# Kernel optimization log

Measured on AMD Instinct MI355X. Metric: run time of the kernel, lower is better.

The kernel has to match this reference:

```python
import jax, jax.numpy as jnp
import numpy as np

TAU = 1.0  # temperature of the NeuralSort relaxation


def _neural_sort(s, tau=TAU):
    """NeuralSort soft permutation matrix for scores s of shape (n,).
    Returns (n, n) row-stochastic matrix; row i ~ one-hot of i-th largest score."""
    n = s.shape[0]
    A_sum = jnp.abs(s[:, None] - s[None, :]).sum(-1)              # (n,)
    scaling = (n + 1 - 2 * jnp.arange(1, n + 1)).astype(s.dtype)  # (n,)
    scores = (scaling[:, None] * s[None, :] - A_sum[None, :]) / tau
    return jax.nn.softmax(scores, axis=-1)


def _soft_perm_gt(events, d):
    """Vectorized version of _get_soft_perm.
    events: (n,) int {0,1}; d: (n,) float durations. Returns (n, n) float32."""
    n = events.shape[0]
    idx = jnp.argsort(d)                 # ascending durations
    e_s = events[idx]                    # events in sorted order
    c = jnp.cumsum(e_s) - e_s            # exclusive event count before position i
    i = jnp.arange(n)
    lo = c                               # first allowed rank column
    hi = jnp.where(e_s == 1, i + 1, n)   # one past last allowed rank column
    j = jnp.arange(n)
    mask = (j[None, :] >= lo[:, None]) & (j[None, :] < hi[:, None])
    rows = mask.astype(jnp.float32) / (hi - lo)[:, None].astype(jnp.float32)
    inv = jnp.argsort(idx)               # perm_un_ascending @ M == rows re-indexed
    return rows[inv]


def _bce(p, y):
    # torch BCELoss: clamp log terms at -100, mean over all elements
    logp = jnp.maximum(jnp.log(p), -100.0)
    log1mp = jnp.maximum(jnp.log1p(-p), -100.0)
    return -(y * logp + (1.0 - y) * log1mp).mean()


def setup_inputs() -> dict:
    key = jax.random.key(0)
    k1, k2, k3 = jax.random.split(key, 3)
    n, C = 2048, 8
    logits = jax.random.normal(k1, (n, C), dtype=jnp.float32)
    durations = jax.random.uniform(k2, (n, C), dtype=jnp.float32)
    events = jax.random.randint(k3, (n, C), 0, 2).astype(jnp.int32)
    return {"logits": logits, "events": events, "durations": durations}


def reference(logits, events, durations):
    def col_loss(lh, e, d):
        p = _neural_sort(lh)        # (n, n) soft permutation prediction
        y = _soft_perm_gt(e, d)     # (n, n) soft permutation label
        return _bce(p, y)

    losses = jax.vmap(col_loss, in_axes=(1, 1, 1))(logits, events, durations)  # (C,)
    m = losses > 0
    denom = jnp.maximum(jnp.sum(m), 1).astype(losses.dtype)
    return jnp.sum(jnp.where(m, losses, 0.0)) / denom
```

## Files before the change

kernel.cpp:

```cpp
#include <hip/hip_runtime.h>
#include <hip/hip_bf16.h>
#include <math.h>

#define N 2048
#define NC 8


#if __has_builtin(__builtin_amdgcn_exp2f)
__device__ __forceinline__ float fexp2(float x) { return __builtin_amdgcn_exp2f(x); }
#else
__device__ __forceinline__ float fexp2(float x) { return exp2f(x); }
#endif
#if __has_builtin(__builtin_amdgcn_logf)
__device__ __forceinline__ float flog2(float x) { return __builtin_amdgcn_logf(x); }
#else
__device__ __forceinline__ float flog2(float x) { return log2f(x); }
#endif

#define INV_LN2 1.4426950408889634f
#define LN2_D   0.6931471805599453
#define CLAMP2  (-144.26950408889634f)

__global__ __launch_bounds__(256) void k_prep(const float* __restrict__ logits,
                                              const float* __restrict__ dur,
                                              const int* __restrict__ ev,
                                              float2* __restrict__ psort,
                                              unsigned short* __restrict__ origj,
                                              int* __restrict__ lohi,
                                              double* __restrict__ acc,
                                              unsigned* __restrict__ counter) {
    __shared__ __align__(16) float s[N];
    __shared__ double part[256];
    __shared__ int pri[256];
    __shared__ __align__(16) unsigned long long keys[N];
    __shared__ int pr[256], pv[256];

    int b = blockIdx.x;
    int tid = threadIdx.x;

    if (b == 0) {
        if (tid < 8) acc[tid] = 0.0;
        else if (tid == 8) counter[0] = 0u;
    }

    if (b < 512) {
        int col = b >> 6, chunk = b & 63;
        for (int k = 0; k < N / 256; ++k) {
            int i = tid + k * 256;
            s[i] = logits[i * NC + col];
        }
        __syncthreads();
        int jl = tid & 31, slice = tid >> 5;
        int j = chunk * 32 + jl;
        float sj = s[j];
        const float4* s4 = (const float4*)(s + slice * 256);
        int ib = slice * 256;
        double a0 = 0.0, a1 = 0.0, a2 = 0.0, a3 = 0.0;
        int rk = 0;
        #pragma unroll 8
        for (int i = 0; i < 64; ++i) {
            float4 q = s4[i];
            int i0 = ib + 4 * i;
            a0 += (double)fabsf(sj - q.x);
            a1 += (double)fabsf(sj - q.y);
            a2 += (double)fabsf(sj - q.z);
            a3 += (double)fabsf(sj - q.w);
            rk += ((int)(q.x < sj)) | (((int)(q.x == sj)) & (int)(i0 + 0 < j));
            rk += ((int)(q.y < sj)) | (((int)(q.y == sj)) & (int)(i0 + 1 < j));
            rk += ((int)(q.z < sj)) | (((int)(q.z == sj)) & (int)(i0 + 2 < j));
            rk += ((int)(q.w < sj)) | (((int)(q.w == sj)) & (int)(i0 + 3 < j));
        }
        part[tid] = (a0 + a1) + (a2 + a3);
        pri[tid] = rk;
        __syncthreads();
        if (tid < 32) {
            double v = ((part[tid]       + part[tid + 32])  + (part[tid + 64]  + part[tid + 96])) +
                       ((part[tid + 128] + part[tid + 160]) + (part[tid + 192] + part[tid + 224]));
            int r = ((pri[tid]       + pri[tid + 32])  + (pri[tid + 64]  + pri[tid + 96])) +
                    ((pri[tid + 128] + pri[tid + 160]) + (pri[tid + 192] + pri[tid + 224]));
            psort[col * N + r] = make_float2(sj * INV_LN2, (float)v * INV_LN2);
            origj[col * N + r] = (unsigned short)j;
        }
    } else {
        int b2 = b - 512;
        int col = b2 >> 6, chunk = b2 & 63;
        for (int k = 0; k < N / 256; ++k) {
            int i = tid + k * 256;
            unsigned int db = __float_as_uint(dur[i * NC + col]);
            int e = ev[i * NC + col];
            keys[i] = ((unsigned long long)db << 32) | (unsigned int)((i << 1) | e);
        }
        __syncthreads();
        int jl = tid & 31, slice = tid >> 5;
        int j = chunk * 32 + jl;
        unsigned long long kj = keys[j];
        const ulonglong2* k2 = (const ulonglong2*)(keys + slice * 256);
        int rank = 0, evlt = 0;
        #pragma unroll 8
        for (int i = 0; i < 128; ++i) {
            ulonglong2 kk = k2[i];
            int lt0 = (kk.x < kj) ? 1 : 0;
            rank += lt0;
            evlt += lt0 & (int)(kk.x & 1ull);
            int lt1 = (kk.y < kj) ? 1 : 0;
            rank += lt1;
            evlt += lt1 & (int)(kk.y & 1ull);
        }
        pr[tid] = rank;
        pv[tid] = evlt;
        __syncthreads();
        if (tid < 32) {
            int r = ((pr[tid]       + pr[tid + 32])  + (pr[tid + 64]  + pr[tid + 96])) +
                    ((pr[tid + 128] + pr[tid + 160]) + (pr[tid + 192] + pr[tid + 224]));
            int v = ((pv[tid]       + pv[tid + 32])  + (pv[tid + 64]  + pv[tid + 96])) +
                    ((pv[tid + 128] + pv[tid + 160]) + (pv[tid + 192] + pv[tid + 224]));
            int e = (int)(kj & 1ull);
            int hi = e ? (r + 1) : N;
            lohi[col * N + j] = v | (hi << 16);
        }
    }
}

__global__ __launch_bounds__(512) void k_bce(const float2* __restrict__ psort,
                                             const unsigned short* __restrict__ origj,
                                             const int* __restrict__ lohi,
                                             double* __restrict__ acc,
                                             unsigned* __restrict__ counter,
                                             float* __restrict__ out) {
    int col = blockIdx.x >> 6;
    int rg  = blockIdx.x & 63;
    __shared__ float4 sa4[N / 2];
    __shared__ unsigned sow[N / 2];
    __shared__ double bsum[8];
    int tid = threadIdx.x;
    int wave = tid >> 6, lane = tid & 63;

    const float4* p4 = (const float4*)(psort + (size_t)col * N);
    const unsigned* g4 = (const unsigned*)(origj + (size_t)col * N);
    #pragma unroll
    for (int k = 0; k < 2; ++k) {
        int i = tid + (k << 9);
        sa4[i] = p4[i];
        sow[i] = g4[i];
    }
    __syncthreads();

    int row0 = (rg << 5) + (wave << 2);
    float sc0 = (float)(N - 1 - 2 * row0);

    int lh[4];
    #pragma unroll
    for (int c = 0; c < 4; ++c) lh[c] = lohi[col * N + row0 + c];

    float m = -INFINITY;
    #pragma unroll
    for (int k = 0; k < 16; ++k) {
        float4 q = sa4[lane + (k << 6)];
        float t0 = fmaf(sc0, q.x, -q.y);
        float t1 = fmaf(sc0, q.z, -q.w);
        m = fmaxf(m, fmaxf(t0, t1));
    }
    #pragma unroll
    for (int off = 32; off > 0; off >>= 1)
        m = fmaxf(m, __shfl_xor(m, off, 64));

    float se0 = 0.0f, se1 = 0.0f, se2 = 0.0f, se3 = 0.0f;
    #pragma unroll
    for (int kg = 0; kg < 2; ++kg) {
        float4 qv[8];
        #pragma unroll
        for (int t = 0; t < 8; ++t)
            qv[t] = sa4[lane + (((kg << 3) | t) << 6)];
        #pragma unroll
        for (int t = 0; t < 8; ++t) {
            float4 q = qv[t];
            float tsa = q.x + q.x;
            float xa0 = fmaf(sc0, q.x, -q.y) - m;
            float xa3 = fmaf(-3.0f, tsa, xa0);
            float tsb = q.z + q.z;
            float xb0 = fmaf(sc0, q.z, -q.w) - m;
            float xb3 = fmaf(-3.0f, tsb, xb0);
            float hi = fmaxf(fmaxf(xa0, xa3), fmaxf(xb0, xb3));
            if (__all(hi < -152.0f)) continue;
            float xa1 = xa0 - tsa;
            float xa2 = fmaf(-2.0f, tsa, xa0);
            float xb1 = xb0 - tsb;
            float xb2 = fmaf(-2.0f, tsb, xb0);
            se0 += fexp2(xa0); se1 += fexp2(xa1); se2 += fexp2(xa2); se3 += fexp2(xa3);
            se0 += fexp2(xb0); se1 += fexp2(xb1); se2 += fexp2(xb2); se3 += fexp2(xb3);
        }
    }
    #pragma unroll
    for (int off = 32; off > 0; off >>= 1) {
        se0 += __shfl_xor(se0, off, 64);
        se1 += __shfl_xor(se1, off, 64);
        se2 += __shfl_xor(se2, off, 64);
        se3 += __shfl_xor(se3, off, 64);
    }
    float se[4] = {se0, se1, se2, se3};

    float L2v[4], C2v[4], yv[4], w2c[4];
    unsigned lo[4], wl[4];
    double rbase = 0.0;
    #pragma unroll
    for (int c = 0; c < 4; ++c) {
        float L2 = flog2(se[c]);
        L2v[c] = L2;
        rbase -= 2048.0 * (double)L2;
        C2v[c] = CLAMP2 + L2;
        w2c[c] = C2v[c] - L2v[c];
        lo[c] = (unsigned)(lh[c] & 0xffff);
        wl[c] = (unsigned)((lh[c] >> 16) & 0xffff) - lo[c];
        yv[c] = 1.0f / (float)wl[c];
    }
    float minL2 = fminf(fminf(L2v[0], L2v[1]), fminf(L2v[2], L2v[3]));
    float C2min = fminf(fminf(C2v[0], C2v[1]), fminf(C2v[2], C2v[3]));
    float tdeep = fminf(C2min, minL2 - 27.0f);
    float t2    = minL2 - 27.0f;

    float a1[4] = {0.0f, 0.0f, 0.0f, 0.0f};
    float a2[4] = {0.0f, 0.0f, 0.0f, 0.0f};
    int cntD[4] = {0, 0, 0, 0};
    int nL = 0;
    #pragma unroll
    for (int kg = 0; kg < 2; ++kg) {
        float4 qv[8];
        unsigned owv[8];
        #pragma unroll
        for (int t = 0; t < 8; ++t) {
            int idx = lane + (((kg << 3) | t) << 6);
            qv[t] = sa4[idx];
            owv[t] = sow[idx];
        }
        #pragma unroll
        for (int t = 0; t < 8; ++t) {
            float4 q = qv[t];
            unsigned ow = owv[t];
            int ja = (int)(ow & 0xffffu), jb = (int)(ow >> 16);
            float tsa = q.x + q.x;
            float xa0 = fmaf(sc0, q.x, -q.y) - m;
            float xa3 = fmaf(-3.0f, tsa, xa0);
            float tsb = q.z + q.z;
            float xb0 = fmaf(sc0, q.z, -q.w) - m;
            float xb3 = fmaf(-3.0f, tsb, xb0);
            float hi = fmaxf(fmaxf(xa0, xa3), fmaxf(xb0, xb3));
            if (__all(hi < tdeep)) {
                ++nL;
                #pragma unroll
                for (int c = 0; c < 4; ++c) {
                    cntD[c] += (int)((unsigned)(ja - lo[c]) < wl[c]);
                    cntD[c] += (int)((unsigned)(jb - lo[c]) < wl[c]);
                }
            } else if (__all(hi < t2)) {
                ++nL;
                {
                    float x = xa0;
                    #pragma unroll
                    for (int c = 0; c < 4; ++c) {
                        float mx1 = fmaxf(x, C2v[c]);
                        float w = ((unsigned)(ja - lo[c]) < wl[c]) ? (mx1 - L2v[c]) : 0.0f;
                        a2[c] += w;
                        x -= tsa;
                    }
                }
                {
                    float x = xb0;
                    #pragma unroll
                    for (int c = 0; c < 4; ++c) {
                        float mx1 = fmaxf(x, C2v[c]);
                        float w = ((unsigned)(jb - lo[c]) < wl[c]) ? (mx1 - L2v[c]) : 0.0f;
                        a2[c] += w;
                        x -= tsb;
                    }
                }
            } else {
                float xav[4], xbv[4];
                xav[0] = xa0; xav[1] = xa0 - tsa;
                xav[2] = fmaf(-2.0f, tsa, xa0); xav[3] = xa3;
                xbv[0] = xb0; xbv[1] = xb0 - tsb;
                xbv[2] = fmaf(-2.0f, tsb, xb0); xbv[3] = xb3;
                float Ea[4], Eb[4];
                #pragma unroll
                for (int c = 0; c < 4; ++c) { Ea[c] = fexp2(xav[c]); Eb[c] = fexp2(xbv[c]); }
                #pragma unroll
                for (int c = 0; c < 4; ++c) {
                    float mx2a = fmaxf(flog2(se[c] - Ea[c]), C2v[c]);
                    a1[c] += mx2a;
                    float mx1a = fmaxf(xav[c], C2v[c]);
                    float wa = ((unsigned)(ja - lo[c]) < wl[c]) ? (mx1a - mx2a) : 0.0f;
                    a2[c] += wa;
                    float mx2b = fmaxf(flog2(se[c] - Eb[c]), C2v[c]);
                    a1[c] += mx2b;
                    float mx1b = fmaxf(xbv[c], C2v[c]);
                    float wb = ((unsigned)(jb - lo[c]) < wl[c]) ? (mx1b - mx2b) : 0.0f;
                    a2[c] += wb;
                }
            }
        }
    }
    float fnL2 = 2.0f * (float)nL;
    #pragma unroll
    for (int c = 0; c < 4; ++c) {
        a1[c] = fmaf(fnL2, L2v[c], a1[c]);
        a2[c] = fmaf((float)cntD[c], w2c[c], a2[c]);
    }
    float r = 0.0f;
    #pragma unroll
    for (int c = 0; c < 4; ++c) r += fmaf(yv[c], a2[c], a1[c]);
    #pragma unroll
    for (int off = 32; off > 0; off >>= 1)
        r += __shfl_xor(r, off, 64);

    if (lane == 0) bsum[wave] = rbase + (double)r;
    __syncthreads();
    if (tid == 0) {
        double tot = ((bsum[0] + bsum[1]) + (bsum[2] + bsum[3])) +
                     ((bsum[4] + bsum[5]) + (bsum[6] + bsum[7]));
        atomicAdd(&acc[col], LN2_D * tot);
        __threadfence();
        unsigned old = atomicAdd(counter, 1u);
        if (old == (unsigned)(NC * 64 - 1)) {
            __threadfence();
            float ssum = 0.0f;
            int cnt = 0;
            for (int c = 0; c < NC; ++c) {
                double av2 = atomicAdd(&acc[c], 0.0);
                float lc = (float)(-av2 / ((double)N * (double)N));
                if (lc > 0.0f) { ssum += lc; cnt++; }
            }
            out[0] = ssum / (float)(cnt > 0 ? cnt : 1);
        }
    }
}

extern "C" void kernel_launch(void* const* d_in, const int* in_sizes, int n_in,
                              void* d_out, int out_size, void* d_ws, size_t ws_size,
                              hipStream_t stream) {
    const float* logits    = (const float*)d_in[0];
    const int*   events    = (const int*)d_in[1];
    const float* durations = (const float*)d_in[2];
    float* out = (float*)d_out;

    char* ws = (char*)d_ws;
    double*         acc     = (double*)ws;
    float2*         psort   = (float2*)(ws + 64);
    int*            lohi    = (int*)(ws + 64 + (size_t)NC * N * sizeof(float2));
    unsigned*       counter = (unsigned*)(ws + 64 + (size_t)NC * N * (sizeof(float2) + sizeof(int)));
    unsigned short* origj   = (unsigned short*)(ws + 64 + (size_t)NC * N * (sizeof(float2) + sizeof(int)) + 64);

    k_prep<<<dim3(1024), 256, 0, stream>>>(logits, durations, events, psort, origj, lohi, acc, counter);
    k_bce<<<dim3(NC * 64), 512, 0, stream>>>(psort, origj, lohi, acc, counter, out);
}
```

Before: 87.96 us.

## Process eight rows per wave in BCE kernel and halve block count

Each wave in the BCE kernel now handles 8 consecutive output rows instead of 4, so each shared-memory load of the sorted scores and indices is reused across twice as many rows. The grid shrinks from 512 to 256 blocks and the completion counter threshold is adjusted to match. The prep kernel's inner loops are also unrolled by 16 instead of 8. The trade-off is more registers per thread and fewer blocks, which on a large GPU may leave compute units idle, and the wider row span means the fast-skip tests are less likely to trigger.

```diff
diff --git a/kernel.cpp b/kernel.cpp
--- a/kernel.cpp
+++ b/kernel.cpp
@@ -57,7 +57,7 @@
         int ib = slice * 256;
         double a0 = 0.0, a1 = 0.0, a2 = 0.0, a3 = 0.0;
         int rk = 0;
-        #pragma unroll 8
+        #pragma unroll 16
         for (int i = 0; i < 64; ++i) {
             float4 q = s4[i];
             int i0 = ib + 4 * i;
@@ -96,7 +96,7 @@
         unsigned long long kj = keys[j];
         const ulonglong2* k2 = (const ulonglong2*)(keys + slice * 256);
         int rank = 0, evlt = 0;
-        #pragma unroll 8
+        #pragma unroll 16
         for (int i = 0; i < 128; ++i) {
             ulonglong2 kk = k2[i];
             int lt0 = (kk.x < kj) ? 1 : 0;
@@ -127,8 +127,8 @@
                                              double* __restrict__ acc,
                                              unsigned* __restrict__ counter,
                                              float* __restrict__ out) {
-    int col = blockIdx.x >> 6;
-    int rg  = blockIdx.x & 63;
+    int col = blockIdx.x >> 5;
+    int rg  = blockIdx.x & 31;
     __shared__ float4 sa4[N / 2];
     __shared__ unsigned sow[N / 2];
     __shared__ double bsum[8];
@@ -145,26 +145,33 @@
     }
     __syncthreads();
 
-    int row0 = (rg << 5) + (wave << 2);
+    int row0 = (rg << 6) + (wave << 3);
     float sc0 = (float)(N - 1 - 2 * row0);
 
-    int lh[4];
-    #pragma unroll
-    for (int c = 0; c < 4; ++c) lh[c] = lohi[col * N + row0 + c];
+    int lh[8];
+    #pragma unroll
+    for (int c = 0; c < 8; ++c) lh[c] = lohi[col * N + row0 + c];
 
     float m = -INFINITY;
     #pragma unroll
-    for (int k = 0; k < 16; ++k) {
-        float4 q = sa4[lane + (k << 6)];
-        float t0 = fmaf(sc0, q.x, -q.y);
-        float t1 = fmaf(sc0, q.z, -q.w);
-        m = fmaxf(m, fmaxf(t0, t1));
+    for (int kg = 0; kg < 2; ++kg) {
+        float4 qv[8];
+        #pragma unroll
+        for (int t = 0; t < 8; ++t)
+            qv[t] = sa4[lane + (((kg << 3) | t) << 6)];
+        #pragma unroll
+        for (int t = 0; t < 8; ++t) {
+            float4 q = qv[t];
+            float t0 = fmaf(sc0, q.x, -q.y);
+            float t1 = fmaf(sc0, q.z, -q.w);
+            m = fmaxf(m, fmaxf(t0, t1));
+        }
     }
     #pragma unroll
     for (int off = 32; off > 0; off >>= 1)
         m = fmaxf(m, __shfl_xor(m, off, 64));
 
-    float se0 = 0.0f, se1 = 0.0f, se2 = 0.0f, se3 = 0.0f;
+    float se[8] = {0.0f, 0.0f, 0.0f, 0.0f, 0.0f, 0.0f, 0.0f, 0.0f};
     #pragma unroll
     for (int kg = 0; kg < 2; ++kg) {
         float4 qv[8];
@@ -176,137 +183,119 @@
             float4 q = qv[t];
             float tsa = q.x + q.x;
             float xa0 = fmaf(sc0, q.x, -q.y) - m;
-            float xa3 = fmaf(-3.0f, tsa, xa0);
+            float xa7 = fmaf(-7.0f, tsa, xa0);
             float tsb = q.z + q.z;
             float xb0 = fmaf(sc0, q.z, -q.w) - m;
-            float xb3 = fmaf(-3.0f, tsb, xb0);
-            float hi = fmaxf(fmaxf(xa0, xa3), fmaxf(xb0, xb3));
+            float xb7 = fmaf(-7.0f, tsb, xb0);
+            float hi = fmaxf(fmaxf(xa0, xa7), fmaxf(xb0, xb7));
             if (__all(hi < -152.0f)) continue;
-            float xa1 = xa0 - tsa;
-            float xa2 = fmaf(-2.0f, tsa, xa0);
-            float xb1 = xb0 - tsb;
-            float xb2 = fmaf(-2.0f, tsb, xb0);
-            se0 += fexp2(xa0); se1 += fexp2(xa1); se2 += fexp2(xa2); se3 += fexp2(xa3);
-            se0 += fexp2(xb0); se1 += fexp2(xb1); se2 += fexp2(xb2); se3 += fexp2(xb3);
-        }
-    }
-    #pragma unroll
-    for (int off = 32; off > 0; off >>= 1) {
-        se0 += __shfl_xor(se0, off, 64);
-        se1 += __shfl_xor(se1, off, 64);
-        se2 += __shfl_xor(se2, off, 64);
-        se3 += __shfl_xor(se3, off, 64);
-    }
-    float se[4] = {se0, se1, se2, se3};
-
-    float L2v[4], C2v[4], yv[4], w2c[4];
-    unsigned lo[4], wl[4];
+            #pragma unroll
+            for (int c = 0; c < 8; ++c) {
+                se[c] += fexp2(fmaf(-(float)c, tsa, xa0));
+                se[c] += fexp2(fmaf(-(float)c, tsb, xb0));
+            }
+        }
+    }
+    #pragma unroll
+    for (int c = 0; c < 8; ++c) {
+        #pragma unroll
+        for (int off = 32; off > 0; off >>= 1)
+            se[c] += __shfl_xor(se[c], off, 64);
+    }
+
+    float L2v[8], C2v[8];
+    unsigned lo[8], wl[8];
     double rbase = 0.0;
     #pragma unroll
-    for (int c = 0; c < 4; ++c) {
+    for (int c = 0; c < 8; ++c) {
         float L2 = flog2(se[c]);
         L2v[c] = L2;
         rbase -= 2048.0 * (double)L2;
         C2v[c] = CLAMP2 + L2;
-        w2c[c] = C2v[c] - L2v[c];
         lo[c] = (unsigned)(lh[c] & 0xffff);
         wl[c] = (unsigned)((lh[c] >> 16) & 0xffff) - lo[c];
-        yv[c] = 1.0f / (float)wl[c];
-    }
-    float minL2 = fminf(fminf(L2v[0], L2v[1]), fminf(L2v[2], L2v[3]));
-    float C2min = fminf(fminf(C2v[0], C2v[1]), fminf(C2v[2], C2v[3]));
+    }
+    float minL2 = L2v[0], C2min = C2v[0];
+    #pragma unroll
+    for (int c = 1; c < 8; ++c) {
+        minL2 = fminf(minL2, L2v[c]);
+        C2min = fminf(C2min, C2v[c]);
+    }
     float tdeep = fminf(C2min, minL2 - 27.0f);
     float t2    = minL2 - 27.0f;
 
-    float a1[4] = {0.0f, 0.0f, 0.0f, 0.0f};
-    float a2[4] = {0.0f, 0.0f, 0.0f, 0.0f};
-    int cntD[4] = {0, 0, 0, 0};
+    float a1[8] = {0.0f, 0.0f, 0.0f, 0.0f, 0.0f, 0.0f, 0.0f, 0.0f};
+    float a2[8] = {0.0f, 0.0f, 0.0f, 0.0f, 0.0f, 0.0f, 0.0f, 0.0f};
+    int cntD[8] = {0, 0, 0, 0, 0, 0, 0, 0};
     int nL = 0;
     #pragma unroll
-    for (int kg = 0; kg < 2; ++kg) {
-        float4 qv[8];
-        unsigned owv[8];
-        #pragma unroll
-        for (int t = 0; t < 8; ++t) {
-            int idx = lane + (((kg << 3) | t) << 6);
-            qv[t] = sa4[idx];
+    for (int kg = 0; kg < 4; ++kg) {
+        float4 qv4[4];
+        unsigned owv[4];
+        #pragma unroll
+        for (int t = 0; t < 4; ++t) {
+            int idx = lane + (((kg << 2) | t) << 6);
+            qv4[t] = sa4[idx];
             owv[t] = sow[idx];
         }
         #pragma unroll
-        for (int t = 0; t < 8; ++t) {
-            float4 q = qv[t];
+        for (int t = 0; t < 4; ++t) {
+            float4 q = qv4[t];
             unsigned ow = owv[t];
             int ja = (int)(ow & 0xffffu), jb = (int)(ow >> 16);
             float tsa = q.x + q.x;
             float xa0 = fmaf(sc0, q.x, -q.y) - m;
-            float xa3 = fmaf(-3.0f, tsa, xa0);
+            float xa7 = fmaf(-7.0f, tsa, xa0);
             float tsb = q.z + q.z;
             float xb0 = fmaf(sc0, q.z, -q.w) - m;
-            float xb3 = fmaf(-3.0f, tsb, xb0);
-            float hi = fmaxf(fmaxf(xa0, xa3), fmaxf(xb0, xb3));
+            float xb7 = fmaf(-7.0f, tsb, xb0);
+            float hi = fmaxf(fmaxf(xa0, xa7), fmaxf(xb0, xb7));
             if (__all(hi < tdeep)) {
                 ++nL;
                 #pragma unroll
-                for (int c = 0; c < 4; ++c) {
+                for (int c = 0; c < 8; ++c) {
                     cntD[c] += (int)((unsigned)(ja - lo[c]) < wl[c]);
                     cntD[c] += (int)((unsigned)(jb - lo[c]) < wl[c]);
                 }
             } else if (__all(hi < t2)) {
                 ++nL;
-                {
-                    float x = xa0;
-                    #pragma unroll
-                    for (int c = 0; c < 4; ++c) {
-                        float mx1 = fmaxf(x, C2v[c]);
-                        float w = ((unsigned)(ja - lo[c]) < wl[c]) ? (mx1 - L2v[c]) : 0.0f;
-                        a2[c] += w;
-                        x -= tsa;
-                    }
-                }
-                {
-                    float x = xb0;
-                    #pragma unroll
-                    for (int c = 0; c < 4; ++c) {
-                        float mx1 = fmaxf(x, C2v[c]);
-                        float w = ((unsigned)(jb - lo[c]) < wl[c]) ? (mx1 - L2v[c]) : 0.0f;
-                        a2[c] += w;
-                        x -= tsb;
-                    }
+                #pragma unroll
+                for (int c = 0; c < 8; ++c) {
+                    float xac = fmaf(-(float)c, tsa, xa0);
+                    float mx1a = fmaxf(xac, C2v[c]);
+                    a2[c] += ((unsigned)(ja - lo[c]) < wl[c]) ? (mx1a - L2v[c]) : 0.0f;
+                    float xbc = fmaf(-(float)c, tsb, xb0);
+                    float mx1b = fmaxf(xbc, C2v[c]);
+                    a2[c] += ((unsigned)(jb - lo[c]) < wl[c]) ? (mx1b - L2v[c]) : 0.0f;
                 }
             } else {
-                float xav[4], xbv[4];
-                xav[0] = xa0; xav[1] = xa0 - tsa;
-                xav[2] = fmaf(-2.0f, tsa, xa0); xav[3] = xa3;
-                xbv[0] = xb0; xbv[1] = xb0 - tsb;
-                xbv[2] = fmaf(-2.0f, tsb, xb0); xbv[3] = xb3;
-                float Ea[4], Eb[4];
                 #pragma unroll
-                for (int c = 0; c < 4; ++c) { Ea[c] = fexp2(xav[c]); Eb[c] = fexp2(xbv[c]); }
-                #pragma unroll
-                for (int c = 0; c < 4; ++c) {
-                    float mx2a = fmaxf(flog2(se[c] - Ea[c]), C2v[c]);
+                for (int c = 0; c < 8; ++c) {
+                    float xac = fmaf(-(float)c, tsa, xa0);
+                    float Ea = fexp2(xac);
+                    float mx2a = fmaxf(flog2(se[c] - Ea), C2v[c]);
                     a1[c] += mx2a;
-                    float mx1a = fmaxf(xav[c], C2v[c]);
-                    float wa = ((unsigned)(ja - lo[c]) < wl[c]) ? (mx1a - mx2a) : 0.0f;
-                    a2[c] += wa;
-                    float mx2b = fmaxf(flog2(se[c] - Eb[c]), C2v[c]);
+                    float mx1a = fmaxf(xac, C2v[c]);
+                    a2[c] += ((unsigned)(ja - lo[c]) < wl[c]) ? (mx1a - mx2a) : 0.0f;
+                    float xbc = fmaf(-(float)c, tsb, xb0);
+                    float Eb = fexp2(xbc);
+                    float mx2b = fmaxf(flog2(se[c] - Eb), C2v[c]);
                     a1[c] += mx2b;
-                    float mx1b = fmaxf(xbv[c], C2v[c]);
-                    float wb = ((unsigned)(jb - lo[c]) < wl[c]) ? (mx1b - mx2b) : 0.0f;
-                    a2[c] += wb;
+                    float mx1b = fmaxf(xbc, C2v[c]);
+                    a2[c] += ((unsigned)(jb - lo[c]) < wl[c]) ? (mx1b - mx2b) : 0.0f;
                 }
             }
         }
     }
     float fnL2 = 2.0f * (float)nL;
-    #pragma unroll
-    for (int c = 0; c < 4; ++c) {
-        a1[c] = fmaf(fnL2, L2v[c], a1[c]);
-        a2[c] = fmaf((float)cntD[c], w2c[c], a2[c]);
-    }
     float r = 0.0f;
     #pragma unroll
-    for (int c = 0; c < 4; ++c) r += fmaf(yv[c], a2[c], a1[c]);
+    for (int c = 0; c < 8; ++c) {
+        float a1c = fmaf(fnL2, L2v[c], a1[c]);
+        float a2c = fmaf((float)cntD[c], C2v[c] - L2v[c], a2[c]);
+        float yvc = 1.0f / (float)wl[c];
+        r += fmaf(yvc, a2c, a1c);
+    }
     #pragma unroll
     for (int off = 32; off > 0; off >>= 1)
         r += __shfl_xor(r, off, 64);
@@ -319,7 +308,7 @@
         atomicAdd(&acc[col], LN2_D * tot);
         __threadfence();
         unsigned old = atomicAdd(counter, 1u);
-        if (old == (unsigned)(NC * 64 - 1)) {
+        if (old == (unsigned)(NC * 32 - 1)) {
             __threadfence();
             float ssum = 0.0f;
             int cnt = 0;
@@ -349,5 +338,5 @@
     unsigned short* origj   = (unsigned short*)(ws + 64 + (size_t)NC * N * (sizeof(float2) + sizeof(int)) + 64);
 
     k_prep<<<dim3(1024), 256, 0, stream>>>(logits, durations, events, psort, origj, lohi, acc, counter);
-    k_bce<<<dim3(NC * 64), 512, 0, stream>>>(psort, origj, lohi, acc, counter, out);
+    k_bce<<<dim3(NC * 32), 512, 0, stream>>>(psort, origj, lohi, acc, counter, out);
 }
```

After: 88.71 us. No clear change (+0.8%).
